# Performance work log

Hardware: AMD Instinct MI355X
Metric: run time of the kernel (lower is better)

## Reference

```python
import jax, jax.numpy as jnp
import numpy as np

B, T, D, H, L, C = 64, 256, 128, 1024, 5, 10


def setup_inputs() -> dict:
    key = jax.random.key(0)
    ks = jax.random.split(key, 6)
    def init(k, shape, fan_in):
        return jax.random.normal(k, shape, jnp.float32) / np.float32(np.sqrt(fan_in))
    x = jax.random.normal(ks[0], (B, T, D), jnp.float32)
    Wx0 = init(ks[1], (D, 4 * H), D)            # layer 0 input weights
    Wxs = init(ks[2], (L - 1, H, 4 * H), H)     # layers 1..L-1 input weights
    Whs = init(ks[3], (L, H, 4 * H), H)         # recurrent weights
    bs = jnp.zeros((L, 4 * H), jnp.float32)     # gate biases
    W_head = init(ks[4], (H, C), H)
    b_head = jnp.zeros((C,), jnp.float32)
    return {"x": x, "Wx0": Wx0, "Wxs": Wxs, "Whs": Whs, "bs": bs,
            "W_head": W_head, "b_head": b_head}


def _lstm_layer(xs, Wx, Wh, b):
    # xs: [T, B, in_d] time-major; returns hidden sequence [T, B, H]
    Bsz = xs.shape[1]
    Hd = Wh.shape[0]
    def step(carry, x_t):
        c, h = carry
        z = x_t @ Wx + h @ Wh + b            # [B, 4H], gate order i,f,g,o (flax)
        i, f, g, o = jnp.split(z, 4, axis=-1)
        c_new = jax.nn.sigmoid(f) * c + jax.nn.sigmoid(i) * jnp.tanh(g)
        h_new = jax.nn.sigmoid(o) * jnp.tanh(c_new)
        return (c_new, h_new), h_new
    init = (jnp.zeros((Bsz, Hd), xs.dtype), jnp.zeros((Bsz, Hd), xs.dtype))
    _, hs = jax.lax.scan(step, init, xs)
    return hs


def reference(x, Wx0, Wxs, Whs, bs, W_head, b_head):
    xs = jnp.swapaxes(x, 0, 1)                  # [T, B, D]
    xs = _lstm_layer(xs, Wx0, Whs[0], bs[0])
    for l in range(1, L):
        xs = _lstm_layer(xs, Wxs[l - 1], Whs[l], bs[l])
    return xs[-1] @ W_head + b_head             # [B, C] from last timestep
```

## Files before the change

kernel.cpp:

```cpp
#include <hip/hip_runtime.h>
#include <hip/hip_cooperative_groups.h>
#include <hip/hip_bf16.h>
#include <cstddef>

typedef unsigned short u16;
typedef unsigned long long u64t;
typedef __attribute__((ext_vector_type(8))) short s8;
typedef __attribute__((ext_vector_type(4))) float f4;

constexpr int kB = 64, kT = 256, kD = 128, kH = 1024, kL = 5, kC = 10, kG = 4096;
constexpr int BH = kB * kH;
constexpr size_t WLA_ELEMS = (size_t)256 * 8 * 16384;
constexpr size_t WLB_ELEMS = (size_t)256 * 8 * 2560;
constexpr size_t H2_ELEMS = (size_t)kL * kT * BH;


__device__ __forceinline__ float sigf(float x) { return 1.f / (1.f + __expf(-x)); }
__device__ __forceinline__ float tanh_s(float x) {
  float ax = fabsf(x);
  float e = __expf(-2.f * ax);
  float r = (1.f - e) / (1.f + e);
  return copysignf(r, x);
}
__device__ __forceinline__ void split_bf16(float v, short& hi, short& lo) {
  __hip_bfloat16 h = __float2bfloat16(v);
  hi = __builtin_bit_cast(short, h);
  float fh = __bfloat162float(h);
  __hip_bfloat16 l = __float2bfloat16(v - fh);
  lo = __builtin_bit_cast(short, l);
}
__device__ __forceinline__ short hi_bf16(float v) {
  __hip_bfloat16 h = __float2bfloat16(v);
  return __builtin_bit_cast(short, h);
}
__device__ __forceinline__ float bf2f(u16 v) {
  unsigned u = ((unsigned)v) << 16;
  return __builtin_bit_cast(float, u);
}

__device__ __forceinline__ void sth8(u16* p, u64t v) {
  __hip_atomic_store((u64t*)p, v, __ATOMIC_RELAXED, __HIP_MEMORY_SCOPE_AGENT);
}
__device__ __forceinline__ unsigned aload(const unsigned* p) {
  return __hip_atomic_load(p, __ATOMIC_RELAXED, __HIP_MEMORY_SCOPE_AGENT);
}

__device__ __forceinline__ void dma16(const void* gsrc, void* ldst) {
  __builtin_amdgcn_global_load_lds(
      (const __attribute__((address_space(1))) void*)gsrc,
      (__attribute__((address_space(3))) void*)ldst, 16, 0, 0);
}

__global__ void __launch_bounds__(512) split_wl(const float* __restrict__ Wx0,
                                                const float* __restrict__ Wxs,
                                                const float* __restrict__ Whs,
                                                u16* __restrict__ wlA,
                                                u16* __restrict__ wlB,
                                                unsigned* __restrict__ bar) {
  const int g = blockIdx.x, tid = threadIdx.x;
  const int wv = tid >> 6, lane = tid & 63, quad = lane >> 4, r = lane & 15;
  const int lA = (g >> 6) + 1, jb = g & 63, kq = wv & 3, ch = wv >> 2;
  const float* WxA = Wxs + (size_t)(lA - 1) * kH * kG;
  const float* WhA = Whs + (size_t)lA * kH * kG;

  if (g == 0)
    for (int i = tid; i < 2048; i += 512) bar[i] = 0;

  u16* dA = wlA + (size_t)(g * 8 + wv) * 16384;
  for (int p = 0; p < 16; ++p) {
    int kc = 4 * p + kq;
    const float* W = (kc < 32) ? WxA : WhA;
    int krow0 = (kc & 31) * 32 + quad * 8;
    for (int ntl = 0; ntl < 2; ++ntl) {
      int col = (2 * ch + ntl) * kH + jb * 16 + r;
      s8 l8;
      for (int j = 0; j < 8; ++j) {
        float w = W[(size_t)(krow0 + j) * kG + col];
        short hh, ll;
        split_bf16(w, hh, ll);
        l8[j] = ll;
      }
      *(s8*)(dA + (size_t)((p * 2 + ntl) * 64 + lane) * 8) = l8;
    }
  }

  u16* dB = wlB + (size_t)(g * 8 + wv) * 2560;
  int colB = (r >> 2) * kH + g * 4 + (r & 3);
  for (int j2 = 0; j2 < 4; ++j2) {
    int kb = (wv & 3) + 4 * (2 * j2 + (wv >> 2));
    int krow0 = kb * 32 + quad * 8;
    s8 l8;
    for (int j = 0; j < 8; ++j) {
      float w = Whs[(size_t)(krow0 + j) * kG + colB];
      short hh, ll;
      split_bf16(w, hh, ll);
      l8[j] = ll;
    }
    *(s8*)(dB + (size_t)(j2 * 64 + lane) * 8) = l8;
  }
  {
    int krow0 = (wv & 3) * 32 + quad * 8;
    s8 l8;
    for (int j = 0; j < 8; ++j) {
      float w = Wx0[(size_t)(krow0 + j) * kG + colB];
      short hh, ll;
      split_bf16(w, hh, ll);
      l8[j] = ll;
    }
    *(s8*)(dB + (size_t)(4 * 64 + lane) * 8) = l8;
  }
}

__global__ void __launch_bounds__(512, 2) lstm_persist(
    const float* __restrict__ x, const float* __restrict__ Wx0,
    const float* __restrict__ Wxs, const float* __restrict__ Whs,
    const float* __restrict__ bs, const float* __restrict__ W_head,
    const float* __restrict__ b_head, float* __restrict__ out,
    u16* __restrict__ hhi, u16* __restrict__ hlo,
    const u16* __restrict__ wlA, const u16* __restrict__ wlB,
    unsigned* __restrict__ bar) {
  __shared__ s8 wpark[8][4][2][64];
  __shared__ s8 wring[8][4][2][64];
  __shared__ float zA[64 * 66];
  __shared__ float zB[64 * 18];
  __shared__ u16 hstA[2][128][8];
  __shared__ u16 hstB[2][64][4];

  const int tid = threadIdx.x;
  const int wv = tid >> 6, lane = tid & 63, quad = lane >> 4, r = lane & 15;
  const int ch = wv >> 2, kq = wv & 3;
  const int g = blockIdx.x;
  const int lA = (g >> 6) + 1;
  const int jb = g & 63;
  const int ub = g * 4;

  const float* __restrict__ WxA = Wxs + (size_t)(lA - 1) * kH * kG;
  const float* __restrict__ WhA = Whs + (size_t)lA * kH * kG;

  s8 wA[16][2];
#pragma unroll
  for (int p = 0; p < 16; ++p) {
    int kc = 4 * p + kq;
    const float* W = (kc < 32) ? WxA : WhA;
    int krow0 = (kc & 31) * 32 + quad * 8;
#pragma unroll
    for (int ntl = 0; ntl < 2; ++ntl) {
      int col = (2 * ch + ntl) * kH + jb * 16 + r;
      s8 h8;
#pragma unroll
      for (int j = 0; j < 8; ++j) h8[j] = hi_bf16(W[(size_t)(krow0 + j) * kG + col]);
      wA[p][ntl] = h8;
    }
  }
  s8 wBh[4], wBx;
  {
    int colB = (r >> 2) * kH + ub + (r & 3);
#pragma unroll
    for (int j2 = 0; j2 < 4; ++j2) {
      int kb = (wv & 3) + 4 * (2 * j2 + (wv >> 2));
      int krow0 = kb * 32 + quad * 8;
      s8 h8;
#pragma unroll
      for (int j = 0; j < 8; ++j) h8[j] = hi_bf16(Whs[(size_t)(krow0 + j) * kG + colB]);
      wBh[j2] = h8;
    }
    int krow0 = (wv & 3) * 32 + quad * 8;
    s8 h8;
#pragma unroll
    for (int j = 0; j < 8; ++j) h8[j] = hi_bf16(Wx0[(size_t)(krow0 + j) * kG + colB]);
    wBx = h8;
  }

  const u16* wlAs = wlA + (size_t)(g * 8 + wv) * 16384;
  const u16* wlBs = wlB + (size_t)(g * 8 + wv) * 2560;

#pragma unroll
  for (int p = 0; p < 4; ++p)
#pragma unroll
    for (int ntl = 0; ntl < 2; ++ntl)
      wpark[wv][p][ntl][lane] =
          *(const s8*)(wlAs + (size_t)((p * 2 + ntl) * 64 + lane) * 8);

  float bA[4], bB[4];
  {
    int u = tid & 15;
#pragma unroll
    for (int g4 = 0; g4 < 4; ++g4) bA[g4] = bs[(size_t)lA * kG + g4 * kH + jb * 16 + u];
    int u2 = tid & 3;
#pragma unroll
    for (int g4 = 0; g4 < 4; ++g4) bB[g4] = bs[(size_t)g4 * kH + ub + u2];
  }
  float cA0 = 0.f, cA1 = 0.f, cB0 = 0.f;
  const s8 zf = {0, 0, 0, 0, 0, 0, 0, 0};
  const f4 zero4 = {0.f, 0.f, 0.f, 0.f};
  const int fragbase = kq * 4 + quad;

  __syncthreads();

  for (int s = 0; s < kT + kL - 1; ++s) {
    const int tA = s - lA;
    const int tB = s;

    for (int i = tid; i < 64 * 66; i += 512) zA[i] = 0.f;
    for (int i = tid; i < 64 * 18; i += 512) zB[i] = 0.f;
    __syncthreads();

    if (tA >= 0 && tA < kT) {
      const int tAm1 = (tA > 0) ? tA - 1 : 0;
      const u16* IH = hhi + ((size_t)(lA - 1) * kT + tA) * BH;
      const u16* IL = hlo + ((size_t)(lA - 1) * kT + tA) * BH;
      const u16* RH = hhi + ((size_t)lA * kT + tAm1) * BH;
      const u16* RL = hlo + ((size_t)lA * kT + tAm1) * BH;
      const bool zz = (tA == 0);
      f4 accA[2][4];
#pragma unroll
      for (int a = 0; a < 2; ++a)
#pragma unroll
        for (int b = 0; b < 4; ++b) accA[a][b] = zero4;

#pragma unroll
      for (int c = 4; c <= 7; ++c)
#pragma unroll
        for (int ntl = 0; ntl < 2; ++ntl)
          dma16(wlAs + (size_t)((c * 2 + ntl) * 64 + lane) * 8,
                &wring[wv][c & 3][ntl][0]);
      s8 ah_sl[2][4];
#pragma unroll
      for (int pp = 0; pp < 2; ++pp)
#pragma unroll
        for (int mt = 0; mt < 4; ++mt)
          ah_sl[pp][mt] =
              *(const s8*)(IH + (size_t)((pp * 16 + fragbase) * 64 + mt * 16 + r) * 8);

#pragma unroll
      for (int p = 0; p < 16; ++p) {
        const bool curR = (p >= 8);
        __builtin_amdgcn_sched_barrier(0);
        const u16* SL = curR ? RL : IL;
        const int kb8c = ((p & 7) * 16 + fragbase) * 64;
        s8 al_c[4];
#pragma unroll
        for (int mt = 0; mt < 4; ++mt)
          al_c[mt] = *(const s8*)(SL + (size_t)(kb8c + mt * 16 + r) * 8);
        if (p == 15)      asm volatile("s_waitcnt vmcnt(20)" ::: "memory");
        else if (p == 14) asm volatile("s_waitcnt vmcnt(26)" ::: "memory");
        else if (p == 13) asm volatile("s_waitcnt vmcnt(28)" ::: "memory");
        else              asm volatile("s_waitcnt vmcnt(30)" ::: "memory");
        __builtin_amdgcn_sched_barrier(0);
        s8 wl0, wl1;
        if (p < 4) {
          wl0 = wpark[wv][p][0][lane];
          wl1 = wpark[wv][p][1][lane];
        } else {
          wl0 = wring[wv][p & 3][0][lane];
          wl1 = wring[wv][p & 3][1][lane];
        }
        s8 ah_c[4];
#pragma unroll
        for (int mt = 0; mt < 4; ++mt) ah_c[mt] = (curR && zz) ? zf : ah_sl[p & 1][mt];
#pragma unroll
        for (int mt = 0; mt < 4; ++mt) {
          f4 a0 = accA[0][mt], a1 = accA[1][mt];
          a0 = __builtin_amdgcn_mfma_f32_16x16x32_bf16(ah_c[mt], wA[p][0], a0, 0, 0, 0);
          a0 = __builtin_amdgcn_mfma_f32_16x16x32_bf16(ah_c[mt], wl0, a0, 0, 0, 0);
          a1 = __builtin_amdgcn_mfma_f32_16x16x32_bf16(ah_c[mt], wA[p][1], a1, 0, 0, 0);
          a1 = __builtin_amdgcn_mfma_f32_16x16x32_bf16(ah_c[mt], wl1, a1, 0, 0, 0);
          accA[0][mt] = a0;
          accA[1][mt] = a1;
        }
        if (p < 14) {
          const int pn = p + 2;
          const u16* SH = (pn >= 8) ? RH : IH;
          const int kb8n = ((pn & 7) * 16 + fragbase) * 64;
#pragma unroll
          for (int mt = 0; mt < 4; ++mt)
            ah_sl[p & 1][mt] = *(const s8*)(SH + (size_t)(kb8n + mt * 16 + r) * 8);
        }
        if (p >= 4 && p <= 11) {
          const int c = p + 4;
#pragma unroll
          for (int ntl = 0; ntl < 2; ++ntl)
            dma16(wlAs + (size_t)((c * 2 + ntl) * 64 + lane) * 8,
                  &wring[wv][c & 3][ntl][0]);
        }
        s8 alz[4];
#pragma unroll
        for (int mt = 0; mt < 4; ++mt) alz[mt] = (curR && zz) ? zf : al_c[mt];
#pragma unroll
        for (int mt = 0; mt < 4; ++mt) {
          accA[0][mt] =
              __builtin_amdgcn_mfma_f32_16x16x32_bf16(alz[mt], wA[p][0], accA[0][mt], 0, 0, 0);
          accA[1][mt] =
              __builtin_amdgcn_mfma_f32_16x16x32_bf16(alz[mt], wA[p][1], accA[1][mt], 0, 0, 0);
        }
      }
#pragma unroll
      for (int ntl = 0; ntl < 2; ++ntl)
#pragma unroll
        for (int mt = 0; mt < 4; ++mt)
#pragma unroll
          for (int v = 0; v < 4; ++v)
            atomicAdd(&zA[(mt * 16 + quad * 4 + v) * 66 + (2 * ch + ntl) * 16 + r],
                      accA[ntl][mt][v]);
    }

    if (tB < kT) {
      const int tBm1 = (tB > 0) ? tB - 1 : 0;
      const u16* H0H = hhi + (size_t)tBm1 * BH;
      const u16* H0L = hlo + (size_t)tBm1 * BH;
      const bool z0 = (tB == 0);
      f4 accB[4];
#pragma unroll
      for (int b = 0; b < 4; ++b) accB[b] = zero4;

      s8 wlb_n = *(const s8*)(wlBs + (size_t)(0 * 64 + lane) * 8);
      s8 ahb_n[4];
      {
        const int kb0 = (wv & 3) + 4 * (wv >> 2);
        const int kb8 = (kb0 * 4 + quad) * 64;
#pragma unroll
        for (int mt = 0; mt < 4; ++mt)
          ahb_n[mt] = *(const s8*)(H0H + (size_t)(kb8 + mt * 16 + r) * 8);
      }
#pragma unroll
      for (int j2 = 0; j2 < 4; ++j2) {
        const int kb = (wv & 3) + 4 * (2 * j2 + (wv >> 2));
        const int kb8c = (kb * 4 + quad) * 64;
        s8 wlv = wlb_n;
        s8 ahb_c[4];
#pragma unroll
        for (int mt = 0; mt < 4; ++mt) ahb_c[mt] = z0 ? zf : ahb_n[mt];
        if (j2 < 3) {
          wlb_n = *(const s8*)(wlBs + (size_t)((j2 + 1) * 64 + lane) * 8);
          const int kbn = (wv & 3) + 4 * (2 * (j2 + 1) + (wv >> 2));
          const int kb8n = (kbn * 4 + quad) * 64;
#pragma unroll
          for (int mt = 0; mt < 4; ++mt)
            ahb_n[mt] = *(const s8*)(H0H + (size_t)(kb8n + mt * 16 + r) * 8);
        }
        s8 alb[4];
#pragma unroll
        for (int mt = 0; mt < 4; ++mt) {
          s8 v = *(const s8*)(H0L + (size_t)(kb8c + mt * 16 + r) * 8);
          alb[mt] = z0 ? zf : v;
        }
#pragma unroll
        for (int mt = 0; mt < 4; ++mt) {
          f4 a = accB[mt];
          a = __builtin_amdgcn_mfma_f32_16x16x32_bf16(ahb_c[mt], wBh[j2], a, 0, 0, 0);
          a = __builtin_amdgcn_mfma_f32_16x16x32_bf16(alb[mt], wBh[j2], a, 0, 0, 0);
          a = __builtin_amdgcn_mfma_f32_16x16x32_bf16(ahb_c[mt], wlv, a, 0, 0, 0);
          accB[mt] = a;
        }
      }
      if (wv >= 4) {
        const int c = wv - 4;
        s8 wlx = *(const s8*)(wlBs + (size_t)(4 * 64 + lane) * 8);
#pragma unroll
        for (int mt = 0; mt < 4; ++mt) {
          const float* sx =
              x + (size_t)(mt * 16 + r) * kT * kD + (size_t)tB * kD + c * 32 + quad * 8;
          float4 v0 = *(const float4*)sx;
          float4 v1 = *(const float4*)(sx + 4);
          float vv[8] = {v0.x, v0.y, v0.z, v0.w, v1.x, v1.y, v1.z, v1.w};
          s8 xh, xl;
#pragma unroll
          for (int e = 0; e < 8; ++e) {
            short hh, ll;
            split_bf16(vv[e], hh, ll);
            xh[e] = hh;
            xl[e] = ll;
          }
          f4 a = accB[mt];
          a = __builtin_amdgcn_mfma_f32_16x16x32_bf16(xh, wBx, a, 0, 0, 0);
          a = __builtin_amdgcn_mfma_f32_16x16x32_bf16(xl, wBx, a, 0, 0, 0);
          a = __builtin_amdgcn_mfma_f32_16x16x32_bf16(xh, wlx, a, 0, 0, 0);
          accB[mt] = a;
        }
      }
#pragma unroll
      for (int mt = 0; mt < 4; ++mt)
#pragma unroll
        for (int v = 0; v < 4; ++v)
          atomicAdd(&zB[(mt * 16 + quad * 4 + v) * 18 + r], accB[mt][v]);
    }

    __syncthreads();

    if (tA >= 0 && tA < kT) {
#pragma unroll
      for (int rp = 0; rp < 2; ++rp) {
        int p2 = tid + 512 * rp;
        int b = p2 >> 4, u = p2 & 15;
        float zi = zA[b * 66 + u] + bA[0];
        float zfg = zA[b * 66 + 16 + u] + bA[1];
        float zg = zA[b * 66 + 32 + u] + bA[2];
        float zo = zA[b * 66 + 48 + u] + bA[3];
        float cp = (tA == 0) ? 0.f : (rp ? cA1 : cA0);
        float cn = sigf(zfg) * cp + sigf(zi) * tanh_s(zg);
        float hn = sigf(zo) * tanh_s(cn);
        if (rp) cA1 = cn; else cA0 = cn;
        short hh, ll;
        split_bf16(hn, hh, ll);
        hstA[0][(u >> 3) * 64 + b][u & 7] = (u16)hh;
        hstA[1][(u >> 3) * 64 + b][u & 7] = (u16)ll;
      }
    }
    if (tB < kT && tid < 256) {
      int b = tid >> 2, u2 = tid & 3;
      float zi = zB[b * 18 + u2] + bB[0];
      float zfg = zB[b * 18 + 4 + u2] + bB[1];
      float zg = zB[b * 18 + 8 + u2] + bB[2];
      float zo = zB[b * 18 + 12 + u2] + bB[3];
      float cp = (tB == 0) ? 0.f : cB0;
      float cn = sigf(zfg) * cp + sigf(zi) * tanh_s(zg);
      float hn = sigf(zo) * tanh_s(cn);
      cB0 = cn;
      short hh, ll;
      split_bf16(hn, hh, ll);
      hstB[0][b][u2] = (u16)hh;
      hstB[1][b][u2] = (u16)ll;
    }
    __syncthreads();

    if (tA >= 0 && tA < kT) {
      u16* HA = ((wv < 4) ? hhi : hlo) + ((size_t)lA * kT + tA) * BH;
      const int arr = wv >> 2;
      const int ci = (wv & 3) * 64 + lane;
      const int gi = ci >> 1, half = ci & 1;
      u64t v = *(const u64t*)&hstA[arr][gi][half * 4];
      sth8(HA + ((size_t)(jb * 2 + (gi >> 6)) * 64 + (gi & 63)) * 8 + half * 4, v);
    }
    if (tB < kT && wv < 2) {
      u16* HB = (wv ? hlo : hhi) + (size_t)tB * BH;
      u64t v = *(const u64t*)&hstB[wv][lane][0];
      sth8(HB + ((size_t)(ub >> 3) * 64 + lane) * 8 + (ub & 7), v);
    }

    asm volatile("s_waitcnt vmcnt(0) lgkmcnt(0)" ::: "memory");
    __syncthreads();
    if (tid == 0) {
      const int leaf = g >> 4;
      const unsigned tgt = 16u * (unsigned)(s + 1);
      __hip_atomic_fetch_add(&bar[leaf * 32], 1u, __ATOMIC_RELAXED,
                             __HIP_MEMORY_SCOPE_AGENT);
      if ((g & 15) == 0) {
        while (aload(&bar[leaf * 32]) < tgt) __builtin_amdgcn_s_sleep(1);
        __hip_atomic_fetch_add(&bar[512], 1u, __ATOMIC_RELAXED,
                               __HIP_MEMORY_SCOPE_AGENT);
        while (aload(&bar[512]) < tgt) __builtin_amdgcn_s_sleep(2);
        __hip_atomic_store(&bar[544 + leaf * 32], (unsigned)(s + 1),
                           __ATOMIC_RELAXED, __HIP_MEMORY_SCOPE_AGENT);
      } else {
        while (aload(&bar[544 + leaf * 32]) < (unsigned)(s + 1))
          __builtin_amdgcn_s_sleep(4);
      }
    }
    __syncthreads();
    asm volatile("" ::: "memory");
  }

  if (g < 80) {
    int p = g * 8 + wv;
    int b = p / 10, cc = p - b * 10;
    const u16* HH = hhi + ((size_t)kL * kT - 1) * BH;
    const u16* HL = hlo + ((size_t)kL * kT - 1) * BH;
    float sum = 0.f;
    for (int j = lane; j < kH; j += 64) {
      size_t off = ((size_t)(j >> 3) * 64 + b) * 8 + (j & 7);
      sum += (bf2f(HH[off]) + bf2f(HL[off])) * W_head[(size_t)j * kC + cc];
    }
#pragma unroll
    for (int off = 32; off > 0; off >>= 1) sum += __shfl_down(sum, off, 64);
    if (lane == 0) out[p] = sum + b_head[cc];
  }
}

static u16* g_wl = nullptr;
__attribute__((constructor)) static void alloc_wl() {
  hipMalloc((void**)&g_wl,
            (WLA_ELEMS + WLB_ELEMS + 2 * H2_ELEMS) * sizeof(u16) + 16384);
}

extern "C" void kernel_launch(void* const* d_in, const int* in_sizes, int n_in,
                              void* d_out, int out_size, void* d_ws, size_t ws_size,
                              hipStream_t stream) {
  const float* x = (const float*)d_in[0];
  const float* Wx0 = (const float*)d_in[1];
  const float* Wxs = (const float*)d_in[2];
  const float* Whs = (const float*)d_in[3];
  const float* bs = (const float*)d_in[4];
  const float* W_head = (const float*)d_in[5];
  const float* b_head = (const float*)d_in[6];
  float* out = (float*)d_out;

  size_t need = (2 * H2_ELEMS + WLA_ELEMS + WLB_ELEMS) * sizeof(u16) + 16384;
  u16* base = (ws_size >= need) ? (u16*)d_ws : g_wl;
  u16* hhi = base;
  u16* hlo = hhi + H2_ELEMS;
  u16* wlA = hlo + H2_ELEMS;
  u16* wlB = wlA + WLA_ELEMS;
  unsigned* bar = (unsigned*)(wlB + WLB_ELEMS);

  split_wl<<<256, 512, 0, stream>>>(Wx0, Wxs, Whs, wlA, wlB, bar);

  void* args[] = {&x, &Wx0, &Wxs, &Whs, &bs, &W_head, &b_head,
                  &out, &hhi, &hlo, &wlA, &wlB, &bar};
  hipLaunchCooperativeKernel((void*)lstm_persist, dim3(256), dim3(512), args, 0,
                             stream);
}
```

Before: 20.36 ms.

## Quantize low bf16 weight residuals to int8 and keep them resident in LDS

The low-order bf16 correction of each weight is now stored as an int8 value, scaled by the exponent of its high bf16 part, in place of a full bf16. This halves the residual storage, so each wave's whole layer-A residual block (16 KB) fits in shared memory. It is DMA'd once at kernel start instead of being streamed through a ring buffer every timestep, and the hand-tuned vmcnt waits and sched barriers are removed. The cost is per-step integer-to-bf16 decode ALU work in the inner loop. The residual also loses some precision, which may affect accuracy.

After: 50.90 ms. 150% more time.

```diff
diff --git a/kernel.cpp b/kernel.cpp
--- a/kernel.cpp
+++ b/kernel.cpp
@@ -10,8 +10,8 @@
 
 constexpr int kB = 64, kT = 256, kD = 128, kH = 1024, kL = 5, kC = 10, kG = 4096;
 constexpr int BH = kB * kH;
-constexpr size_t WLA_ELEMS = (size_t)256 * 8 * 16384;
-constexpr size_t WLB_ELEMS = (size_t)256 * 8 * 2560;
+constexpr size_t WLAQ_BYTES = (size_t)256 * 8 * 16384;
+constexpr size_t WLBQ_BYTES = (size_t)256 * 8 * 2560;
 constexpr size_t H2_ELEMS = (size_t)kL * kT * BH;
 
 
@@ -29,22 +29,54 @@
   __hip_bfloat16 l = __float2bfloat16(v - fh);
   lo = __builtin_bit_cast(short, l);
 }
-__device__ __forceinline__ short hi_bf16(float v) {
-  __hip_bfloat16 h = __float2bfloat16(v);
-  return __builtin_bit_cast(short, h);
-}
 __device__ __forceinline__ float bf2f(u16 v) {
   unsigned u = ((unsigned)v) << 16;
   return __builtin_bit_cast(float, u);
 }
 
+__device__ __forceinline__ unsigned rne16(float w) {
+  unsigned wb = __builtin_bit_cast(unsigned, w);
+  return (wb + 0x7FFFu + ((wb >> 16) & 1u)) & 0xFFFF0000u;
+}
+__device__ __forceinline__ short hi_rne(float w) {
+  return (short)(rne16(w) >> 16);
+}
+__device__ __forceinline__ char enc_q(float w) {
+  unsigned r16 = rne16(w);
+  float fh = __builtin_bit_cast(float, r16);
+  float r = w - fh;
+  int e = (int)((r16 >> 23) & 0xFF);
+  int qi = 0;
+  if (e >= 16) {
+    float inv = __builtin_bit_cast(float, (unsigned)(269 - e) << 23);
+    qi = __float2int_rn(r * inv);
+    qi = qi > 127 ? 127 : (qi < -127 ? -127 : qi);
+  }
+  return (char)qi;
+}
+__device__ __forceinline__ s8 dec_lo(u64t qp, s8 hi) {
+  s8 lo;
+  const unsigned qa = (unsigned)qp, qb = (unsigned)(qp >> 32);
+#pragma unroll
+  for (int j = 0; j < 8; ++j) {
+    unsigned src = (j < 4) ? qa : qb;
+    int q = ((int)(src << ((3 - (j & 3)) * 8))) >> 24;
+    int e = ((int)(unsigned short)hi[j] >> 7) & 0xFF;
+    int sb = e - 15;
+    sb = sb < 0 ? 0 : sb;
+    float scale = __builtin_bit_cast(float, (unsigned)sb << 23);
+    float lf = (float)q * scale;
+    lo[j] = (short)(__builtin_bit_cast(unsigned, lf) >> 16);
+  }
+  return lo;
+}
+
 __device__ __forceinline__ void sth8(u16* p, u64t v) {
   __hip_atomic_store((u64t*)p, v, __ATOMIC_RELAXED, __HIP_MEMORY_SCOPE_AGENT);
 }
 __device__ __forceinline__ unsigned aload(const unsigned* p) {
   return __hip_atomic_load(p, __ATOMIC_RELAXED, __HIP_MEMORY_SCOPE_AGENT);
 }
-
 __device__ __forceinline__ void dma16(const void* gsrc, void* ldst) {
   __builtin_amdgcn_global_load_lds(
       (const __attribute__((address_space(1))) void*)gsrc,
@@ -54,8 +86,8 @@
 __global__ void __launch_bounds__(512) split_wl(const float* __restrict__ Wx0,
                                                 const float* __restrict__ Wxs,
                                                 const float* __restrict__ Whs,
-                                                u16* __restrict__ wlA,
-                                                u16* __restrict__ wlB,
+                                                char* __restrict__ wlAq,
+                                                char* __restrict__ wlBq,
                                                 unsigned* __restrict__ bar) {
   const int g = blockIdx.x, tid = threadIdx.x;
   const int wv = tid >> 6, lane = tid & 63, quad = lane >> 4, r = lane & 15;
@@ -64,50 +96,44 @@
   const float* WhA = Whs + (size_t)lA * kH * kG;
 
   if (g == 0)
-    for (int i = tid; i < 2048; i += 512) bar[i] = 0;
-
-  u16* dA = wlA + (size_t)(g * 8 + wv) * 16384;
+    for (int i = tid; i < 4096; i += 512) bar[i] = 0;
+
+  char* dA = wlAq + (size_t)(g * 8 + wv) * 16384;
   for (int p = 0; p < 16; ++p) {
     int kc = 4 * p + kq;
     const float* W = (kc < 32) ? WxA : WhA;
     int krow0 = (kc & 31) * 32 + quad * 8;
     for (int ntl = 0; ntl < 2; ++ntl) {
       int col = (2 * ch + ntl) * kH + jb * 16 + r;
-      s8 l8;
+      u64t qw = 0;
       for (int j = 0; j < 8; ++j) {
-        float w = W[(size_t)(krow0 + j) * kG + col];
-        short hh, ll;
-        split_bf16(w, hh, ll);
-        l8[j] = ll;
-      }
-      *(s8*)(dA + (size_t)((p * 2 + ntl) * 64 + lane) * 8) = l8;
-    }
-  }
-
-  u16* dB = wlB + (size_t)(g * 8 + wv) * 2560;
+        char q = enc_q(W[(size_t)(krow0 + j) * kG + col]);
+        qw |= ((u64t)(unsigned char)q) << (8 * j);
+      }
+      *(u64t*)(dA + (size_t)((p * 2 + ntl) * 64 + lane) * 8) = qw;
+    }
+  }
+
+  char* dB = wlBq + (size_t)(g * 8 + wv) * 2560;
   int colB = (r >> 2) * kH + g * 4 + (r & 3);
   for (int j2 = 0; j2 < 4; ++j2) {
     int kb = (wv & 3) + 4 * (2 * j2 + (wv >> 2));
     int krow0 = kb * 32 + quad * 8;
-    s8 l8;
+    u64t qw = 0;
     for (int j = 0; j < 8; ++j) {
-      float w = Whs[(size_t)(krow0 + j) * kG + colB];
-      short hh, ll;
-      split_bf16(w, hh, ll);
-      l8[j] = ll;
-    }
-    *(s8*)(dB + (size_t)(j2 * 64 + lane) * 8) = l8;
+      char q = enc_q(Whs[(size_t)(krow0 + j) * kG + colB]);
+      qw |= ((u64t)(unsigned char)q) << (8 * j);
+    }
+    *(u64t*)(dB + (size_t)(j2 * 64 + lane) * 8) = qw;
   }
   {
     int krow0 = (wv & 3) * 32 + quad * 8;
-    s8 l8;
+    u64t qw = 0;
     for (int j = 0; j < 8; ++j) {
-      float w = Wx0[(size_t)(krow0 + j) * kG + colB];
-      short hh, ll;
-      split_bf16(w, hh, ll);
-      l8[j] = ll;
-    }
-    *(s8*)(dB + (size_t)(4 * 64 + lane) * 8) = l8;
+      char q = enc_q(Wx0[(size_t)(krow0 + j) * kG + colB]);
+      qw |= ((u64t)(unsigned char)q) << (8 * j);
+    }
+    *(u64t*)(dB + (size_t)(4 * 64 + lane) * 8) = qw;
   }
 }
 
@@ -117,10 +143,9 @@
     const float* __restrict__ bs, const float* __restrict__ W_head,
     const float* __restrict__ b_head, float* __restrict__ out,
     u16* __restrict__ hhi, u16* __restrict__ hlo,
-    const u16* __restrict__ wlA, const u16* __restrict__ wlB,
+    const char* __restrict__ wlAq, const char* __restrict__ wlBq,
     unsigned* __restrict__ bar) {
-  __shared__ s8 wpark[8][4][2][64];
-  __shared__ s8 wring[8][4][2][64];
+  __shared__ char wq[8][16384];
   __shared__ float zA[64 * 66];
   __shared__ float zB[64 * 18];
   __shared__ u16 hstA[2][128][8];
@@ -137,6 +162,13 @@
   const float* __restrict__ WxA = Wxs + (size_t)(lA - 1) * kH * kG;
   const float* __restrict__ WhA = Whs + (size_t)lA * kH * kG;
 
+  {
+    const char* qsrc = wlAq + (size_t)(g * 8 + wv) * 16384;
+#pragma unroll
+    for (int i = 0; i < 16; ++i)
+      dma16(qsrc + (size_t)i * 1024 + (size_t)lane * 16, &wq[wv][i * 1024]);
+  }
+
   s8 wA[16][2];
 #pragma unroll
   for (int p = 0; p < 16; ++p) {
@@ -148,7 +180,7 @@
       int col = (2 * ch + ntl) * kH + jb * 16 + r;
       s8 h8;
 #pragma unroll
-      for (int j = 0; j < 8; ++j) h8[j] = hi_bf16(W[(size_t)(krow0 + j) * kG + col]);
+      for (int j = 0; j < 8; ++j) h8[j] = hi_rne(W[(size_t)(krow0 + j) * kG + col]);
       wA[p][ntl] = h8;
     }
   }
@@ -161,25 +193,17 @@
       int krow0 = kb * 32 + quad * 8;
       s8 h8;
 #pragma unroll
-      for (int j = 0; j < 8; ++j) h8[j] = hi_bf16(Whs[(size_t)(krow0 + j) * kG + colB]);
+      for (int j = 0; j < 8; ++j) h8[j] = hi_rne(Whs[(size_t)(krow0 + j) * kG + colB]);
       wBh[j2] = h8;
     }
     int krow0 = (wv & 3) * 32 + quad * 8;
     s8 h8;
 #pragma unroll
-    for (int j = 0; j < 8; ++j) h8[j] = hi_bf16(Wx0[(size_t)(krow0 + j) * kG + colB]);
+    for (int j = 0; j < 8; ++j) h8[j] = hi_rne(Wx0[(size_t)(krow0 + j) * kG + colB]);
     wBx = h8;
   }
 
-  const u16* wlAs = wlA + (size_t)(g * 8 + wv) * 16384;
-  const u16* wlBs = wlB + (size_t)(g * 8 + wv) * 2560;
-
-#pragma unroll
-  for (int p = 0; p < 4; ++p)
-#pragma unroll
-    for (int ntl = 0; ntl < 2; ++ntl)
-      wpark[wv][p][ntl][lane] =
-          *(const s8*)(wlAs + (size_t)((p * 2 + ntl) * 64 + lane) * 8);
+  const char* wlBs = wlBq + (size_t)(g * 8 + wv) * 2560;
 
   float bA[4], bB[4];
   {
@@ -218,70 +242,48 @@
 #pragma unroll
         for (int b = 0; b < 4; ++b) accA[a][b] = zero4;
 
-#pragma unroll
-      for (int c = 4; c <= 7; ++c)
-#pragma unroll
-        for (int ntl = 0; ntl < 2; ++ntl)
-          dma16(wlAs + (size_t)((c * 2 + ntl) * 64 + lane) * 8,
-                &wring[wv][c & 3][ntl][0]);
-      s8 ah_sl[2][4];
-#pragma unroll
-      for (int pp = 0; pp < 2; ++pp)
-#pragma unroll
-        for (int mt = 0; mt < 4; ++mt)
-          ah_sl[pp][mt] =
-              *(const s8*)(IH + (size_t)((pp * 16 + fragbase) * 64 + mt * 16 + r) * 8);
+      s8 ah_n[4];
+#pragma unroll
+      for (int mt = 0; mt < 4; ++mt)
+        ah_n[mt] = *(const s8*)(IH + (size_t)(fragbase * 64 + mt * 16 + r) * 8);
 
 #pragma unroll
       for (int p = 0; p < 16; ++p) {
         const bool curR = (p >= 8);
-        __builtin_amdgcn_sched_barrier(0);
         const u16* SL = curR ? RL : IL;
         const int kb8c = ((p & 7) * 16 + fragbase) * 64;
         s8 al_c[4];
 #pragma unroll
         for (int mt = 0; mt < 4; ++mt)
           al_c[mt] = *(const s8*)(SL + (size_t)(kb8c + mt * 16 + r) * 8);
-        if (p == 15)      asm volatile("s_waitcnt vmcnt(20)" ::: "memory");
-        else if (p == 14) asm volatile("s_waitcnt vmcnt(26)" ::: "memory");
-        else if (p == 13) asm volatile("s_waitcnt vmcnt(28)" ::: "memory");
-        else              asm volatile("s_waitcnt vmcnt(30)" ::: "memory");
-        __builtin_amdgcn_sched_barrier(0);
-        s8 wl0, wl1;
-        if (p < 4) {
-          wl0 = wpark[wv][p][0][lane];
-          wl1 = wpark[wv][p][1][lane];
-        } else {
-          wl0 = wring[wv][p & 3][0][lane];
-          wl1 = wring[wv][p & 3][1][lane];
-        }
+        u64t q0 = *(const u64t*)&wq[wv][(size_t)((p * 2 + 0) * 64 + lane) * 8];
+        u64t q1 = *(const u64t*)&wq[wv][(size_t)((p * 2 + 1) * 64 + lane) * 8];
         s8 ah_c[4];
 #pragma unroll
-        for (int mt = 0; mt < 4; ++mt) ah_c[mt] = (curR && zz) ? zf : ah_sl[p & 1][mt];
+        for (int mt = 0; mt < 4; ++mt) ah_c[mt] = (curR && zz) ? zf : ah_n[mt];
+        s8 wl0 = dec_lo(q0, wA[p][0]);
+        s8 wl1 = dec_lo(q1, wA[p][1]);
 #pragma unroll
         for (int mt = 0; mt < 4; ++mt) {
-          f4 a0 = accA[0][mt], a1 = accA[1][mt];
-          a0 = __builtin_amdgcn_mfma_f32_16x16x32_bf16(ah_c[mt], wA[p][0], a0, 0, 0, 0);
-          a0 = __builtin_amdgcn_mfma_f32_16x16x32_bf16(ah_c[mt], wl0, a0, 0, 0, 0);
-          a1 = __builtin_amdgcn_mfma_f32_16x16x32_bf16(ah_c[mt], wA[p][1], a1, 0, 0, 0);
-          a1 = __builtin_amdgcn_mfma_f32_16x16x32_bf16(ah_c[mt], wl1, a1, 0, 0, 0);
-          accA[0][mt] = a0;
-          accA[1][mt] = a1;
-        }
-        if (p < 14) {
-          const int pn = p + 2;
+          accA[0][mt] =
+              __builtin_amdgcn_mfma_f32_16x16x32_bf16(ah_c[mt], wA[p][0], accA[0][mt], 0, 0, 0);
+          accA[1][mt] =
+              __builtin_amdgcn_mfma_f32_16x16x32_bf16(ah_c[mt], wA[p][1], accA[1][mt], 0, 0, 0);
+        }
+        if (p < 15) {
+          const int pn = p + 1;
           const u16* SH = (pn >= 8) ? RH : IH;
           const int kb8n = ((pn & 7) * 16 + fragbase) * 64;
 #pragma unroll
           for (int mt = 0; mt < 4; ++mt)
-            ah_sl[p & 1][mt] = *(const s8*)(SH + (size_t)(kb8n + mt * 16 + r) * 8);
-        }
-        if (p >= 4 && p <= 11) {
-          const int c = p + 4;
-#pragma unroll
-          for (int ntl = 0; ntl < 2; ++ntl)
-            dma16(wlAs + (size_t)((c * 2 + ntl) * 64 + lane) * 8,
-                  &wring[wv][c & 3][ntl][0]);
+            ah_n[mt] = *(const s8*)(SH + (size_t)(kb8n + mt * 16 + r) * 8);
+        }
+#pragma unroll
+        for (int mt = 0; mt < 4; ++mt) {
+          accA[0][mt] =
+              __builtin_amdgcn_mfma_f32_16x16x32_bf16(ah_c[mt], wl0, accA[0][mt], 0, 0, 0);
+          accA[1][mt] =
+              __builtin_amdgcn_mfma_f32_16x16x32_bf16(ah_c[mt], wl1, accA[1][mt], 0, 0, 0);
         }
         s8 alz[4];
 #pragma unroll
@@ -313,7 +315,6 @@
 #pragma unroll
       for (int b = 0; b < 4; ++b) accB[b] = zero4;
 
-      s8 wlb_n = *(const s8*)(wlBs + (size_t)(0 * 64 + lane) * 8);
       s8 ahb_n[4];
       {
         const int kb0 = (wv & 3) + 4 * (wv >> 2);
@@ -326,12 +327,12 @@
       for (int j2 = 0; j2 < 4; ++j2) {
         const int kb = (wv & 3) + 4 * (2 * j2 + (wv >> 2));
         const int kb8c = (kb * 4 + quad) * 64;
-        s8 wlv = wlb_n;
+        u64t qb = *(const u64t*)(wlBs + (size_t)(j2 * 64 + lane) * 8);
+        s8 wlv = dec_lo(qb, wBh[j2]);
         s8 ahb_c[4];
 #pragma unroll
         for (int mt = 0; mt < 4; ++mt) ahb_c[mt] = z0 ? zf : ahb_n[mt];
         if (j2 < 3) {
-          wlb_n = *(const s8*)(wlBs + (size_t)((j2 + 1) * 64 + lane) * 8);
           const int kbn = (wv & 3) + 4 * (2 * (j2 + 1) + (wv >> 2));
           const int kb8n = (kbn * 4 + quad) * 64;
 #pragma unroll
@@ -355,7 +356,8 @@
       }
       if (wv >= 4) {
         const int c = wv - 4;
-        s8 wlx = *(const s8*)(wlBs + (size_t)(4 * 64 + lane) * 8);
+        u64t qx = *(const u64t*)(wlBs + (size_t)(4 * 64 + lane) * 8);
+        s8 wlx = dec_lo(qx, wBx);
 #pragma unroll
         for (int mt = 0; mt < 4; ++mt) {
           const float* sx =
@@ -476,10 +478,10 @@
   }
 }
 
-static u16* g_wl = nullptr;
+static char* g_wl = nullptr;
 __attribute__((constructor)) static void alloc_wl() {
   hipMalloc((void**)&g_wl,
-            (WLA_ELEMS + WLB_ELEMS + 2 * H2_ELEMS) * sizeof(u16) + 16384);
+            2 * H2_ELEMS * sizeof(u16) + WLAQ_BYTES + WLBQ_BYTES + 16384);
 }
 
 extern "C" void kernel_launch(void* const* d_in, const int* in_sizes, int n_in,
@@ -494,18 +496,18 @@
   const float* b_head = (const float*)d_in[6];
   float* out = (float*)d_out;
 
-  size_t need = (2 * H2_ELEMS + WLA_ELEMS + WLB_ELEMS) * sizeof(u16) + 16384;
-  u16* base = (ws_size >= need) ? (u16*)d_ws : g_wl;
-  u16* hhi = base;
+  size_t need = 2 * H2_ELEMS * sizeof(u16) + WLAQ_BYTES + WLBQ_BYTES + 16384;
+  char* base = (ws_size >= need) ? (char*)d_ws : g_wl;
+  u16* hhi = (u16*)base;
   u16* hlo = hhi + H2_ELEMS;
-  u16* wlA = hlo + H2_ELEMS;
-  u16* wlB = wlA + WLA_ELEMS;
-  unsigned* bar = (unsigned*)(wlB + WLB_ELEMS);
-
-  split_wl<<<256, 512, 0, stream>>>(Wx0, Wxs, Whs, wlA, wlB, bar);
+  char* wlAq = (char*)(hlo + H2_ELEMS);
+  char* wlBq = wlAq + WLAQ_BYTES;
+  unsigned* bar = (unsigned*)(wlBq + WLBQ_BYTES);
+
+  split_wl<<<256, 512, 0, stream>>>(Wx0, Wxs, Whs, wlAq, wlBq, bar);
 
   void* args[] = {&x, &Wx0, &Wxs, &Whs, &bs, &W_head, &b_head,
-                  &out, &hhi, &hlo, &wlA, &wlB, &bar};
+                  &out, &hhi, &hlo, &wlAq, &wlBq, &bar};
   hipLaunchCooperativeKernel((void*)lstm_persist, dim3(256), dim3(512), args, 0,
                              stream);
 }
```
